# Kernel tuning notes

Measured on AMD Instinct MI355X. Metric: run time of the kernel, lower is better.

Reference implementation:

```python
import jax, jax.numpy as jnp
import numpy as np

E = 8          # num_global_experts
K = 2          # top-k
D = 1024       # model_dim
H = 4096       # hidden_size_per_expert
CAP_FACTOR = 1.0


def setup_inputs() -> dict:
    key = jax.random.key(0)
    ks = jax.random.split(key, 5)
    x = jax.random.normal(ks[0], (4, 2048, D), jnp.float32)
    gate_w = jax.random.normal(ks[1], (E, D), jnp.float32) * 0.02
    fc1_w = jax.random.normal(ks[2], (E, H, D), jnp.float32) * 0.02
    fc1_b = jnp.zeros((E, 1, H), jnp.float32)
    fc2_w = jax.random.normal(ks[3], (E, H, D), jnp.float32) * 0.02
    fc2_b = jnp.zeros((E, 1, D), jnp.float32)
    return {"x": x, "gate_w": gate_w, "fc1_w": fc1_w, "fc1_b": fc1_b,
            "fc2_w": fc2_w, "fc2_b": fc2_b}


def reference(x, gate_w, fc1_w, fc1_b, fc2_w, fc2_b):
    B, S, Dm = x.shape
    xf = x.reshape(-1, Dm)                       # [N, D] tokens
    N = xf.shape[0]
    cap = int(K * CAP_FACTOR * ((N + E - 1) // E))  # expert capacity

    # ---- gating (top-k softmax, normalized) ----
    logits = xf @ gate_w.T                       # [N, E]
    scores = jax.nn.softmax(logits, axis=-1)
    topv, topi = jax.lax.top_k(scores, K)        # [N, K]
    gates = topv / jnp.sum(topv, axis=-1, keepdims=True)

    # ---- per-slot locations within each expert (sequential over K slots) ----
    offset = jnp.zeros((E,), jnp.int32)
    locs = []
    for j in range(K):
        mask = jax.nn.one_hot(topi[:, j], E, dtype=jnp.int32)   # [N, E]
        loc_in = jnp.cumsum(mask, axis=0) - 1 + offset[None, :]
        locs.append(jnp.take_along_axis(loc_in, topi[:, j:j + 1], axis=1)[:, 0])
        offset = offset + mask.sum(axis=0)
    loc = jnp.stack(locs, axis=1)                # [N, K]
    valid = loc < cap                            # capacity-dropped tokens
    flat_idx = jnp.where(valid, topi * cap + loc, 0)   # [N, K]
    w = valid.astype(xf.dtype)

    # ---- dispatch (scatter tokens into [E, cap, D], postscore => unweighted) ----
    disp = jnp.zeros((E * cap, Dm), xf.dtype)
    disp = disp.at[flat_idx.reshape(-1)].add(
        (xf[:, None, :] * w[:, :, None]).reshape(-1, Dm))
    de = disp.reshape(E, cap, Dm)

    # ---- batched expert FFN: relu(x @ fc1^T + b1) @ fc2 + b2 ----
    h = jax.nn.relu(jnp.einsum('ecd,ehd->ech', de, fc1_w) + fc1_b)
    eo = jnp.einsum('ech,ehd->ecd', h, fc2_w) + fc2_b

    # ---- combine (gather + gate-weighted sum over K slots) ----
    gathered = eo.reshape(E * cap, Dm)[flat_idx]       # [N, K, D]
    out = jnp.sum(gathered * (gates * w)[:, :, None], axis=1)
    return out.reshape(B, S, Dm)
```

## Files before the change

kernel.cpp:

```cpp
#include <hip/hip_runtime.h>
#include <hip/hip_bf16.h>
#include <stdint.h>

#define NEXP 8
#define DM   1024
#define HID  4096
#define NTOK 8192
#define CAPS 2048

#define BM 256
#define BN 256
#define BK 64

typedef __attribute__((ext_vector_type(8))) short bh8_t;
typedef __attribute__((ext_vector_type(4))) float f32x4_t;
typedef unsigned short u16;

static __device__ __forceinline__ u16 f2bf(float f) {
    __hip_bfloat16 h = __float2bfloat16(f);
    return __builtin_bit_cast(u16, h);
}
static __device__ __forceinline__ float bf2f(u16 u) {
    unsigned int x = ((unsigned int)u) << 16;
    return __builtin_bit_cast(float, x);
}

#define FENCE asm volatile("" ::: "memory")
#define BAR   do { FENCE; __builtin_amdgcn_s_barrier(); FENCE; } while (0)
#define LGKM0 do { asm volatile("s_waitcnt lgkmcnt(0)" ::: "memory"); \
                   __builtin_amdgcn_sched_barrier(0); } while (0)
#define MFMA(d, a, b) d = __builtin_amdgcn_mfma_f32_16x16x32_bf16(a, b, d, 0, 0, 0)

__global__ __launch_bounds__(256) void k_conv_bf16(const float* __restrict__ in,
                                                   u16* __restrict__ out, long n) {
    long i = ((long)blockIdx.x * 256 + threadIdx.x) * 4;
    if (i >= n) return;
    float4 v = *(const float4*)(in + i);
    ushort4 o;
    o.x = f2bf(v.x); o.y = f2bf(v.y); o.z = f2bf(v.z); o.w = f2bf(v.w);
    *(ushort4*)(out + i) = o;
}

__global__ __launch_bounds__(256) void k_transpose_w2(const float* __restrict__ in,
                                                      u16* __restrict__ out) {
    int e = blockIdx.z;
    const float* I = in + (long)e * HID * DM;
    u16* O = out + (long)e * DM * HID;
    __shared__ float t[32][33];
    int x = threadIdx.x & 31, y = threadIdx.x >> 5;
    int h0 = blockIdx.x * 32, d0 = blockIdx.y * 32;
    #pragma unroll
    for (int i = 0; i < 4; ++i)
        t[y + 8*i][x] = I[(long)(h0 + y + 8*i) * DM + d0 + x];
    __syncthreads();
    #pragma unroll
    for (int i = 0; i < 4; ++i)
        O[(long)(d0 + y + 8*i) * HID + h0 + x] = f2bf(t[x][y + 8*i]);
}

__global__ __launch_bounds__(256) void k_gating(const float* __restrict__ x,
        const float* __restrict__ gw, int* __restrict__ topi, float* __restrict__ gates) {
    __shared__ float sg[NEXP][DM];
    int tid = threadIdx.x;
    for (int i = tid; i < NEXP*DM; i += 256) ((float*)sg)[i] = gw[i];
    __syncthreads();
    int lane = tid & 63, w = tid >> 6;
    long n = (long)blockIdx.x * 4 + w;
    const float* xr = x + n * DM;
    float acc[NEXP] = {};
    for (int i = 0; i < DM/64; ++i) {
        float xv = xr[lane + i*64];
        #pragma unroll
        for (int e = 0; e < NEXP; ++e) acc[e] += xv * sg[e][lane + i*64];
    }
    #pragma unroll
    for (int e = 0; e < NEXP; ++e)
        #pragma unroll
        for (int off = 32; off; off >>= 1) acc[e] += __shfl_xor(acc[e], off);
    if (lane == 0) {
        float mx = acc[0];
        #pragma unroll
        for (int e = 1; e < NEXP; ++e) mx = fmaxf(mx, acc[e]);
        float p[NEXP];
        #pragma unroll
        for (int e = 0; e < NEXP; ++e) p[e] = expf(acc[e] - mx);
        float v0 = p[0]; int i0 = 0;
        #pragma unroll
        for (int e = 1; e < NEXP; ++e) if (p[e] > v0) { v0 = p[e]; i0 = e; }
        float v1 = -1.f; int i1 = 0;
        #pragma unroll
        for (int e = 0; e < NEXP; ++e) if (e != i0 && p[e] > v1) { v1 = p[e]; i1 = e; }
        float tot = v0 + v1;
        topi[n*2]   = i0; topi[n*2+1] = i1;
        gates[n*2]  = v0 / tot; gates[n*2+1] = v1 / tot;
    }
}

__global__ __launch_bounds__(64) void k_locate(const int* __restrict__ topi,
                                               int* __restrict__ flat) {
    int lane = threadIdx.x;
    const int TPL = NTOK / 64;
    int base = lane * TPL;
    int offset[NEXP];
    #pragma unroll
    for (int e = 0; e < NEXP; ++e) offset[e] = 0;
    for (int j = 0; j < 2; ++j) {
        unsigned long long pk = 0;
        for (int t = 0; t < TPL; ++t) {
            int e = topi[(long)(base + t)*2 + j];
            pk += 1ull << (8*e);
        }
        int cnt[NEXP], excl[NEXP];
        #pragma unroll
        for (int e = 0; e < NEXP; ++e) cnt[e] = (int)((pk >> (8*e)) & 0xff);
        #pragma unroll
        for (int e = 0; e < NEXP; ++e) {
            int v = cnt[e];
            for (int d = 1; d < 64; d <<= 1) {
                int o = __shfl_up(v, d);
                if (lane >= d) v += o;
            }
            excl[e] = v - cnt[e] + offset[e];
            offset[e] += __shfl(v, 63);
        }
        unsigned long long lo = 0, hi = 0;
        #pragma unroll
        for (int e = 0; e < 4; ++e)    lo |= (unsigned long long)(excl[e] & 0xffff) << (16*e);
        #pragma unroll
        for (int e = 4; e < NEXP; ++e) hi |= (unsigned long long)(excl[e] & 0xffff) << (16*(e-4));
        for (int t = 0; t < TPL; ++t) {
            long n = base + t;
            int e = topi[n*2 + j];
            int sh = 16 * (e & 3);
            int loc;
            if (e < 4) { loc = (int)((lo >> sh) & 0xffff); lo += 1ull << sh; }
            else       { loc = (int)((hi >> sh) & 0xffff); hi += 1ull << sh; }
            flat[n*2 + j] = (loc < CAPS) ? (e * CAPS + loc) : -1;
        }
    }
}

__global__ __launch_bounds__(256) void k_dispatch(const float* __restrict__ x,
        const int* __restrict__ flat, u16* __restrict__ disp) {
    long n = blockIdx.x;
    int tid = threadIdx.x;
    float4 v = *(const float4*)(x + n*DM + tid*4);
    ushort4 o; o.x = f2bf(v.x); o.y = f2bf(v.y); o.z = f2bf(v.z); o.w = f2bf(v.w);
    int f0 = flat[n*2], f1 = flat[n*2+1];
    if (f0 >= 0) *(ushort4*)(disp + (long)f0*DM + tid*4) = o;
    if (f1 >= 0) *(ushort4*)(disp + (long)f1*DM + tid*4) = o;
}

static __device__ __forceinline__ void stage_half(const u16* __restrict__ g, int ld,
                                                  u16* R, int wid, int lane) {
    int rlo = wid*8 + (lane >> 3);
    int cbe = ((lane & 7) ^ ((lane >> 3) & 7)) * 8;
    const u16* s0 = g + (long)rlo * ld + cbe;
    const u16* s1 = g + (long)(rlo + 64) * ld + cbe;
    u16* d0 = R + wid*512 + lane*8;
    u16* d1 = R + 4096 + wid*512 + lane*8;
    __builtin_amdgcn_global_load_lds((const __attribute__((address_space(1))) void*)s0,
        (__attribute__((address_space(3))) void*)d0, 16, 0, 0);
    __builtin_amdgcn_global_load_lds((const __attribute__((address_space(1))) void*)s1,
        (__attribute__((address_space(3))) void*)d1, 16, 0, 0);
}

template<int RELU>
__global__ __launch_bounds__(512, 2)
void k_gemm8(const u16* __restrict__ A, const u16* __restrict__ B,
             const float* __restrict__ bias, u16* __restrict__ C,
             int N, int K, long strA, long strB, long strBias, long strC)
{
    __shared__ u16 sm[2][2][2][8192];

    int gx = gridDim.x, gy = gridDim.y;
    int nwg = gx * gy * (int)gridDim.z;
    int lin = blockIdx.x + gx * (blockIdx.y + gy * blockIdx.z);
    int qq  = nwg >> 3;
    int swz = (lin & 7) * qq + (lin >> 3);
    int gxy = gx * gy;
    int bz = swz / gxy, rm = swz % gxy, by = rm / gx, bx = rm % gx;

    const u16* Ae = A + (long)bz * strA;
    const u16* Be = B + (long)bz * strB;
    const float* bi = bias + (long)bz * strBias;
    u16* Ce = C + (long)bz * strC;

    long tm = (long)by * BM, tn = (long)bx * BN;
    const u16* Abase = Ae + tm * (long)K;
    const u16* Bbase = Be + tn * (long)K;

    int tid = threadIdx.x, lane = tid & 63, wid = tid >> 6;
    int wr = wid >> 2, wc = wid & 3;

    int frow = lane & 15;
    int fc0 = (((lane >> 4) * 16)      ^ ((lane & 7) << 4)) >> 1;
    int fc1 = ((64 + (lane >> 4) * 16) ^ ((lane & 7) << 4)) >> 1;

    const int NT = K / BK;

    f32x4_t acc[8][4] = {};

    auto STG = [&](int buf, int ab, int half, int kt) {
        const u16* g = (ab ? Bbase : Abase) + (long)(half * 128) * K + (long)kt * BK;
        stage_half(g, K, &sm[buf][ab][half][0], wid, lane);
    };
    auto LDA = [&](int c, int mi, int kk) -> bh8_t {
        const u16* p = &sm[c][0][wr][0] + (mi * 16 + frow) * 64 + (kk ? fc1 : fc0);
        return *(const bh8_t*)p;
    };
    auto LDB = [&](int c, int ni, int kk) -> bh8_t {
        const u16* p = &sm[c][1][wc >> 1][0] + ((wc & 1) * 64 + ni * 16 + frow) * 64 + (kk ? fc1 : fc0);
        return *(const bh8_t*)p;
    };

    auto ktile = [&](int c, int kt, int s12, int s34, int vm) {
        bh8_t a0[4][2], a1[4][2], bf[4][2];
        #pragma unroll
        for (int mi = 0; mi < 4; ++mi) { a0[mi][0] = LDA(c, mi, 0); a0[mi][1] = LDA(c, mi, 1); }
        #pragma unroll
        for (int ni = 0; ni < 2; ++ni) { bf[ni][0] = LDB(c, ni, 0); bf[ni][1] = LDB(c, ni, 1); }
        if (s12) STG(c ^ 1, 0, 1, kt + 1);
        BAR; LGKM0;
        __builtin_amdgcn_s_setprio(1);
        #pragma unroll
        for (int mi = 0; mi < 4; ++mi)
            #pragma unroll
            for (int ni = 0; ni < 2; ++ni)
                #pragma unroll
                for (int kk = 0; kk < 2; ++kk) MFMA(acc[mi][ni], a0[mi][kk], bf[ni][kk]);
        __builtin_amdgcn_s_setprio(0);
        __builtin_amdgcn_sched_barrier(0);
        BAR;
        #pragma unroll
        for (int ni = 2; ni < 4; ++ni) { bf[ni][0] = LDB(c, ni, 0); bf[ni][1] = LDB(c, ni, 1); }
        if (s12) STG(c ^ 1, 1, 1, kt + 1);
        BAR; LGKM0;
        __builtin_amdgcn_s_setprio(1);
        #pragma unroll
        for (int mi = 0; mi < 4; ++mi)
            #pragma unroll
            for (int ni = 2; ni < 4; ++ni)
                #pragma unroll
                for (int kk = 0; kk < 2; ++kk) MFMA(acc[mi][ni], a0[mi][kk], bf[ni][kk]);
        __builtin_amdgcn_s_setprio(0);
        __builtin_amdgcn_sched_barrier(0);
        BAR;
        #pragma unroll
        for (int mi = 0; mi < 4; ++mi) { a1[mi][0] = LDA(c, mi + 4, 0); a1[mi][1] = LDA(c, mi + 4, 1); }
        if (s34) STG(c, 1, 0, kt + 2);
        BAR; LGKM0;
        __builtin_amdgcn_s_setprio(1);
        #pragma unroll
        for (int mi = 0; mi < 4; ++mi)
            #pragma unroll
            for (int ni = 0; ni < 2; ++ni)
                #pragma unroll
                for (int kk = 0; kk < 2; ++kk) MFMA(acc[mi + 4][ni], a1[mi][kk], bf[ni][kk]);
        __builtin_amdgcn_s_setprio(0);
        __builtin_amdgcn_sched_barrier(0);
        BAR;
        if (s34) STG(c, 0, 0, kt + 2);
        if (vm == 4)      { asm volatile("s_waitcnt vmcnt(4)" ::: "memory"); }
        else if (vm == 0) { asm volatile("s_waitcnt vmcnt(0)" ::: "memory"); }
        BAR; LGKM0;
        __builtin_amdgcn_s_setprio(1);
        #pragma unroll
        for (int mi = 0; mi < 4; ++mi)
            #pragma unroll
            for (int ni = 2; ni < 4; ++ni)
                #pragma unroll
                for (int kk = 0; kk < 2; ++kk) MFMA(acc[mi + 4][ni], a1[mi][kk], bf[ni][kk]);
        __builtin_amdgcn_s_setprio(0);
        __builtin_amdgcn_sched_barrier(0);
        BAR;
    };

    STG(0, 0, 0, 0); STG(0, 0, 1, 0); STG(0, 1, 0, 0); STG(0, 1, 1, 0);
    STG(1, 1, 0, 1); STG(1, 0, 0, 1);
    asm volatile("s_waitcnt vmcnt(4)" ::: "memory");
    BAR;

    int kt = 0;
    for (; kt < NT - 2; ++kt) ktile(kt & 1, kt, 1, 1, 4);
    ktile(kt & 1, kt, 1, 0, 0); ++kt;
    ktile(kt & 1, kt, 0, 0, -1);

    u16* wb = &sm[0][0][0][0] + wid * 8192;
    #pragma unroll
    for (int mi = 0; mi < 8; ++mi)
        #pragma unroll
        for (int ni = 0; ni < 4; ++ni) {
            float bv = bi[tn + wc * 64 + ni * 16 + (lane & 15)];
            #pragma unroll
            for (int r = 0; r < 4; ++r) {
                int row = mi * 16 + (lane >> 4) * 4 + r;
                int ce  = ni * 16 + (lane & 15);
                float v = acc[mi][ni][r] + bv;
                if (RELU) v = fmaxf(v, 0.f);
                wb[row * 64 + (ce ^ ((row & 7) << 3))] = f2bf(v);
            }
        }
    __syncthreads();
    long crow = tm + wr * 128;
    long ccol = tn + wc * 64 + (lane & 7) * 8;
    #pragma unroll
    for (int i = 0; i < 16; ++i) {
        int rr = i * 8 + (lane >> 3);
        bh8_t v = *(const bh8_t*)(wb + rr * 64 + (((lane & 7) * 8) ^ ((rr & 7) << 3)));
        *(bh8_t*)(Ce + (crow + rr) * N + ccol) = v;
    }
}

__global__ __launch_bounds__(256) void k_combine(const u16* __restrict__ eo,
        const int* __restrict__ flat, const float* __restrict__ gates,
        float* __restrict__ out) {
    long n = blockIdx.x;
    int tid = threadIdx.x;
    int f0 = flat[n*2], f1 = flat[n*2+1];
    float g0 = (f0 >= 0) ? gates[n*2]   : 0.f;
    float g1 = (f1 >= 0) ? gates[n*2+1] : 0.f;
    const u16* r0 = eo + (long)(f0 >= 0 ? f0 : 0) * DM;
    const u16* r1 = eo + (long)(f1 >= 0 ? f1 : 0) * DM;
    ushort4 a = *(const ushort4*)(r0 + tid*4);
    ushort4 b = *(const ushort4*)(r1 + tid*4);
    float4 o;
    o.x = g0*bf2f(a.x) + g1*bf2f(b.x);
    o.y = g0*bf2f(a.y) + g1*bf2f(b.y);
    o.z = g0*bf2f(a.z) + g1*bf2f(b.z);
    o.w = g0*bf2f(a.w) + g1*bf2f(b.w);
    *(float4*)(out + n*DM + tid*4) = o;
}

extern "C" void kernel_launch(void* const* d_in, const int* in_sizes, int n_in,
                              void* d_out, int out_size, void* d_ws, size_t ws_size,
                              hipStream_t stream) {
    const float* x    = (const float*)d_in[0];
    const float* gw   = (const float*)d_in[1];
    const float* fc1w = (const float*)d_in[2];
    const float* fc1b = (const float*)d_in[3];
    const float* fc2w = (const float*)d_in[4];
    const float* fc2b = (const float*)d_in[5];
    float* out = (float*)d_out;
    char* ws = (char*)d_ws;

    u16* disp = (u16*)(ws);
    u16* eo   = disp;
    u16* h    = (u16*)(ws + 33554432L);
    u16* w1b  = (u16*)(ws + 33554432L + 134217728L);
    u16* w2t  = (u16*)(ws + 33554432L + 134217728L + 67108864L);
    char* tail = ws + 33554432L + 134217728L + 67108864L + 67108864L;
    int*   topi  = (int*)tail;
    float* gates = (float*)(tail + 65536);
    int*   flat  = (int*)(tail + 131072);

    long n1 = (long)NEXP * HID * DM;

    hipMemsetAsync(disp, 0, (size_t)NEXP * CAPS * DM * 2, stream);
    k_conv_bf16<<<dim3(n1/1024), 256, 0, stream>>>(fc1w, w1b, n1);
    k_transpose_w2<<<dim3(HID/32, DM/32, NEXP), 256, 0, stream>>>(fc2w, w2t);
    k_gating<<<dim3(NTOK/4), 256, 0, stream>>>(x, gw, topi, gates);
    k_locate<<<dim3(1), 64, 0, stream>>>(topi, flat);
    k_dispatch<<<dim3(NTOK), 256, 0, stream>>>(x, flat, disp);
    k_gemm8<1><<<dim3(HID/BN, CAPS/BM, NEXP), 512, 0, stream>>>(
        disp, w1b, fc1b, h, HID, DM,
        (long)CAPS*DM, (long)HID*DM, (long)HID, (long)CAPS*HID);
    k_gemm8<0><<<dim3(DM/BN, CAPS/BM, NEXP), 512, 0, stream>>>(
        h, w2t, fc2b, eo, DM, HID,
        (long)CAPS*HID, (long)DM*HID, (long)DM, (long)CAPS*DM);
    k_combine<<<dim3(NTOK), 256, 0, stream>>>(eo, flat, gates, out);
}
```

Before: 471.9 us.

## Fuse fc1 weight bf16 conversion into GEMM loads, widen transpose, drop memset

Removes the standalone fp32-to-bf16 conversion pass over fc1 weights. The first expert GEMM now loads fp32 B tiles into registers, converts them, and writes them swizzled into LDS within a reworked software pipeline. The fc2 transpose kernel moves to 64x64 tiles with float4 loads and 16-byte bf16 stores, and the zeroing memset of the dispatch buffer is dropped. In exchange, GEMM1 reads twice the B bytes for every tile it reuses across row blocks and adds conversion ALU work and register pressure. It also relies on never-gathered capacity slots not mattering.

```diff
diff --git a/kernel.cpp b/kernel.cpp
--- a/kernel.cpp
+++ b/kernel.cpp
@@ -29,33 +29,36 @@
 #define BAR   do { FENCE; __builtin_amdgcn_s_barrier(); FENCE; } while (0)
 #define LGKM0 do { asm volatile("s_waitcnt lgkmcnt(0)" ::: "memory"); \
                    __builtin_amdgcn_sched_barrier(0); } while (0)
+#define SB0   __builtin_amdgcn_sched_barrier(0)
 #define MFMA(d, a, b) d = __builtin_amdgcn_mfma_f32_16x16x32_bf16(a, b, d, 0, 0, 0)
-
-__global__ __launch_bounds__(256) void k_conv_bf16(const float* __restrict__ in,
-                                                   u16* __restrict__ out, long n) {
-    long i = ((long)blockIdx.x * 256 + threadIdx.x) * 4;
-    if (i >= n) return;
-    float4 v = *(const float4*)(in + i);
-    ushort4 o;
-    o.x = f2bf(v.x); o.y = f2bf(v.y); o.z = f2bf(v.z); o.w = f2bf(v.w);
-    *(ushort4*)(out + i) = o;
-}
 
 __global__ __launch_bounds__(256) void k_transpose_w2(const float* __restrict__ in,
                                                       u16* __restrict__ out) {
     int e = blockIdx.z;
     const float* I = in + (long)e * HID * DM;
     u16* O = out + (long)e * DM * HID;
-    __shared__ float t[32][33];
-    int x = threadIdx.x & 31, y = threadIdx.x >> 5;
-    int h0 = blockIdx.x * 32, d0 = blockIdx.y * 32;
-    #pragma unroll
-    for (int i = 0; i < 4; ++i)
-        t[y + 8*i][x] = I[(long)(h0 + y + 8*i) * DM + d0 + x];
+    __shared__ float t[64][65];
+    int h0 = blockIdx.x * 64, d0 = blockIdx.y * 64;
+    int tid = threadIdx.x;
+    int r = tid >> 4, cw = (tid & 15) * 4;
+    #pragma unroll
+    for (int i = 0; i < 4; ++i) {
+        float4 v = *(const float4*)(I + (long)(h0 + r + 16*i) * DM + d0 + cw);
+        t[r + 16*i][cw]     = v.x;
+        t[r + 16*i][cw + 1] = v.y;
+        t[r + 16*i][cw + 2] = v.z;
+        t[r + 16*i][cw + 3] = v.w;
+    }
     __syncthreads();
-    #pragma unroll
-    for (int i = 0; i < 4; ++i)
-        O[(long)(d0 + y + 8*i) * HID + h0 + x] = f2bf(t[x][y + 8*i]);
+    int dl = tid >> 2, hc = (tid & 3) * 16;
+    bh8_t w0, w1;
+    #pragma unroll
+    for (int j = 0; j < 8; ++j) w0[j] = (short)f2bf(t[hc + j][dl]);
+    #pragma unroll
+    for (int j = 0; j < 8; ++j) w1[j] = (short)f2bf(t[hc + 8 + j][dl]);
+    u16* o = O + (long)(d0 + dl) * HID + h0 + hc;
+    *(bh8_t*)o = w0;
+    *(bh8_t*)(o + 8) = w1;
 }
 
 __global__ __launch_bounds__(256) void k_gating(const float* __restrict__ x,
@@ -165,9 +168,11 @@
         (__attribute__((address_space(3))) void*)d1, 16, 0, 0);
 }
 
-template<int RELU>
+struct Bregs { float4 a0, a1, b0, b1; };
+
+template<int RELU, int BF32>
 __global__ __launch_bounds__(512, 2)
-void k_gemm8(const u16* __restrict__ A, const u16* __restrict__ B,
+void k_gemm8(const u16* __restrict__ A, const void* __restrict__ Bv,
              const float* __restrict__ bias, u16* __restrict__ C,
              int N, int K, long strA, long strB, long strBias, long strC)
 {
@@ -182,13 +187,15 @@
     int bz = swz / gxy, rm = swz % gxy, by = rm / gx, bx = rm % gx;
 
     const u16* Ae = A + (long)bz * strA;
-    const u16* Be = B + (long)bz * strB;
     const float* bi = bias + (long)bz * strBias;
     u16* Ce = C + (long)bz * strC;
 
     long tm = (long)by * BM, tn = (long)bx * BN;
     const u16* Abase = Ae + tm * (long)K;
-    const u16* Bbase = Be + tn * (long)K;
+    const u16*   Bbase16 = nullptr;
+    const float* Bbase32 = nullptr;
+    if constexpr (BF32) Bbase32 = (const float*)Bv + (long)bz * strB + tn * (long)K;
+    else                Bbase16 = (const u16*)Bv  + (long)bz * strB + tn * (long)K;
 
     int tid = threadIdx.x, lane = tid & 63, wid = tid >> 6;
     int wr = wid >> 2, wc = wid & 3;
@@ -197,13 +204,36 @@
     int fc0 = (((lane >> 4) * 16)      ^ ((lane & 7) << 4)) >> 1;
     int fc1 = ((64 + (lane >> 4) * 16) ^ ((lane & 7) << 4)) >> 1;
 
+    int rlo = wid*8 + (lane >> 3);
+    int c0  = (lane & 7) * 8;
+
     const int NT = K / BK;
 
     f32x4_t acc[8][4] = {};
 
     auto STG = [&](int buf, int ab, int half, int kt) {
-        const u16* g = (ab ? Bbase : Abase) + (long)(half * 128) * K + (long)kt * BK;
+        const u16* g = (ab ? Bbase16 : Abase) + (long)(half * 128) * K + (long)kt * BK;
         stage_half(g, K, &sm[buf][ab][half][0], wid, lane);
+    };
+    auto LBLD = [&](int half, int kt) -> Bregs {
+        const float* g  = Bbase32 + (long)(half * 128 + rlo) * K + (long)kt * BK + c0;
+        const float* g2 = g + 64L * K;
+        Bregs r;
+        r.a0 = *(const float4*)g;  r.a1 = *(const float4*)(g + 4);
+        r.b0 = *(const float4*)g2; r.b1 = *(const float4*)(g2 + 4);
+        return r;
+    };
+    auto BWR = [&](int buf, int half, const Bregs& v) {
+        u16* R = &sm[buf][1][half][0];
+        int key = (rlo & 7) << 3;
+        u16* d1 = R + rlo * 64 + (c0 ^ key);
+        u16* d2 = R + (rlo + 64) * 64 + (c0 ^ key);
+        bh8_t w1, w2;
+        w1[0]=(short)f2bf(v.a0.x); w1[1]=(short)f2bf(v.a0.y); w1[2]=(short)f2bf(v.a0.z); w1[3]=(short)f2bf(v.a0.w);
+        w1[4]=(short)f2bf(v.a1.x); w1[5]=(short)f2bf(v.a1.y); w1[6]=(short)f2bf(v.a1.z); w1[7]=(short)f2bf(v.a1.w);
+        w2[0]=(short)f2bf(v.b0.x); w2[1]=(short)f2bf(v.b0.y); w2[2]=(short)f2bf(v.b0.z); w2[3]=(short)f2bf(v.b0.w);
+        w2[4]=(short)f2bf(v.b1.x); w2[5]=(short)f2bf(v.b1.y); w2[6]=(short)f2bf(v.b1.z); w2[7]=(short)f2bf(v.b1.w);
+        *(bh8_t*)d1 = w1; *(bh8_t*)d2 = w2;
     };
     auto LDA = [&](int c, int mi, int kk) -> bh8_t {
         const u16* p = &sm[c][0][wr][0] + (mi * 16 + frow) * 64 + (kk ? fc1 : fc0);
@@ -214,7 +244,7 @@
         return *(const bh8_t*)p;
     };
 
-    auto ktile = [&](int c, int kt, int s12, int s34, int vm) {
+    auto ktile16 = [&](int c, int kt, int s12, int s34, int vm) {
         bh8_t a0[4][2], a1[4][2], bf[4][2];
         #pragma unroll
         for (int mi = 0; mi < 4; ++mi) { a0[mi][0] = LDA(c, mi, 0); a0[mi][1] = LDA(c, mi, 1); }
@@ -229,9 +259,7 @@
             for (int ni = 0; ni < 2; ++ni)
                 #pragma unroll
                 for (int kk = 0; kk < 2; ++kk) MFMA(acc[mi][ni], a0[mi][kk], bf[ni][kk]);
-        __builtin_amdgcn_s_setprio(0);
-        __builtin_amdgcn_sched_barrier(0);
-        BAR;
+        __builtin_amdgcn_s_setprio(0); SB0; BAR;
         #pragma unroll
         for (int ni = 2; ni < 4; ++ni) { bf[ni][0] = LDB(c, ni, 0); bf[ni][1] = LDB(c, ni, 1); }
         if (s12) STG(c ^ 1, 1, 1, kt + 1);
@@ -243,9 +271,7 @@
             for (int ni = 2; ni < 4; ++ni)
                 #pragma unroll
                 for (int kk = 0; kk < 2; ++kk) MFMA(acc[mi][ni], a0[mi][kk], bf[ni][kk]);
-        __builtin_amdgcn_s_setprio(0);
-        __builtin_amdgcn_sched_barrier(0);
-        BAR;
+        __builtin_amdgcn_s_setprio(0); SB0; BAR;
         #pragma unroll
         for (int mi = 0; mi < 4; ++mi) { a1[mi][0] = LDA(c, mi + 4, 0); a1[mi][1] = LDA(c, mi + 4, 1); }
         if (s34) STG(c, 1, 0, kt + 2);
@@ -257,9 +283,7 @@
             for (int ni = 0; ni < 2; ++ni)
                 #pragma unroll
                 for (int kk = 0; kk < 2; ++kk) MFMA(acc[mi + 4][ni], a1[mi][kk], bf[ni][kk]);
-        __builtin_amdgcn_s_setprio(0);
-        __builtin_amdgcn_sched_barrier(0);
-        BAR;
+        __builtin_amdgcn_s_setprio(0); SB0; BAR;
         if (s34) STG(c, 0, 0, kt + 2);
         if (vm == 4)      { asm volatile("s_waitcnt vmcnt(4)" ::: "memory"); }
         else if (vm == 0) { asm volatile("s_waitcnt vmcnt(0)" ::: "memory"); }
@@ -271,20 +295,105 @@
             for (int ni = 2; ni < 4; ++ni)
                 #pragma unroll
                 for (int kk = 0; kk < 2; ++kk) MFMA(acc[mi + 4][ni], a1[mi][kk], bf[ni][kk]);
-        __builtin_amdgcn_s_setprio(0);
-        __builtin_amdgcn_sched_barrier(0);
+        __builtin_amdgcn_s_setprio(0); SB0; BAR;
+    };
+
+    auto ktile32 = [&](int c, int kt, int s12, int s34) {
+        bh8_t a0[4][2], a1[4][2], bf[4][2];
+        Bregs lb1, lb0;
+        #pragma unroll
+        for (int mi = 0; mi < 4; ++mi) { a0[mi][0] = LDA(c, mi, 0); a0[mi][1] = LDA(c, mi, 1); }
+        #pragma unroll
+        for (int ni = 0; ni < 2; ++ni) { bf[ni][0] = LDB(c, ni, 0); bf[ni][1] = LDB(c, ni, 1); }
+        SB0;
+        if (s12) lb1 = LBLD(1, kt + 1);
+        SB0;
+        if (s34) lb0 = LBLD(0, kt + 2);
+        SB0;
+        if (s12) STG(c ^ 1, 0, 1, kt + 1);
+        BAR; LGKM0;
+        __builtin_amdgcn_s_setprio(1);
+        #pragma unroll
+        for (int mi = 0; mi < 4; ++mi)
+            #pragma unroll
+            for (int ni = 0; ni < 2; ++ni)
+                #pragma unroll
+                for (int kk = 0; kk < 2; ++kk) MFMA(acc[mi][ni], a0[mi][kk], bf[ni][kk]);
+        __builtin_amdgcn_s_setprio(0); SB0; BAR;
+        #pragma unroll
+        for (int ni = 2; ni < 4; ++ni) { bf[ni][0] = LDB(c, ni, 0); bf[ni][1] = LDB(c, ni, 1); }
+        BAR; LGKM0;
+        __builtin_amdgcn_s_setprio(1);
+        #pragma unroll
+        for (int mi = 0; mi < 4; ++mi)
+            #pragma unroll
+            for (int ni = 2; ni < 4; ++ni)
+                #pragma unroll
+                for (int kk = 0; kk < 2; ++kk) MFMA(acc[mi][ni], a0[mi][kk], bf[ni][kk]);
+        __builtin_amdgcn_s_setprio(0); SB0; BAR;
+        #pragma unroll
+        for (int mi = 0; mi < 4; ++mi) { a1[mi][0] = LDA(c, mi + 4, 0); a1[mi][1] = LDA(c, mi + 4, 1); }
+        SB0;
+        if (s12) {
+            if (s34) { asm volatile("s_waitcnt vmcnt(6)" ::: "memory"); }
+            else     { asm volatile("s_waitcnt vmcnt(2)" ::: "memory"); }
+            BWR(c ^ 1, 1, lb1);
+        }
+        BAR; LGKM0;
+        __builtin_amdgcn_s_setprio(1);
+        #pragma unroll
+        for (int mi = 0; mi < 4; ++mi)
+            #pragma unroll
+            for (int ni = 0; ni < 2; ++ni)
+                #pragma unroll
+                for (int kk = 0; kk < 2; ++kk) MFMA(acc[mi + 4][ni], a1[mi][kk], bf[ni][kk]);
+        __builtin_amdgcn_s_setprio(0); SB0; BAR;
+        if (s34) {
+            asm volatile("s_waitcnt vmcnt(2)" ::: "memory");
+            BWR(c, 0, lb0);
+            SB0;
+            STG(c, 0, 0, kt + 2);
+            SB0;
+        }
+        if (s12) {
+            if (s34) { asm volatile("s_waitcnt vmcnt(2)" ::: "memory"); }
+            else     { asm volatile("s_waitcnt vmcnt(0)" ::: "memory"); }
+        }
+        BAR; LGKM0;
+        __builtin_amdgcn_s_setprio(1);
+        #pragma unroll
+        for (int mi = 0; mi < 4; ++mi)
+            #pragma unroll
+            for (int ni = 2; ni < 4; ++ni)
+                #pragma unroll
+                for (int kk = 0; kk < 2; ++kk) MFMA(acc[mi + 4][ni], a1[mi][kk], bf[ni][kk]);
+        __builtin_amdgcn_s_setprio(0); SB0; BAR;
+    };
+
+    if constexpr (BF32) {
+        Bregs t0 = LBLD(0, 0);
+        asm volatile("s_waitcnt vmcnt(0)" ::: "memory"); BWR(0, 0, t0);
+        Bregs t1 = LBLD(1, 0);
+        asm volatile("s_waitcnt vmcnt(0)" ::: "memory"); BWR(0, 1, t1);
+        Bregs t2 = LBLD(0, 1);
+        asm volatile("s_waitcnt vmcnt(0)" ::: "memory"); BWR(1, 0, t2);
+        STG(0, 0, 0, 0); STG(0, 0, 1, 0); STG(1, 0, 0, 1);
+        asm volatile("s_waitcnt vmcnt(0) lgkmcnt(0)" ::: "memory");
         BAR;
-    };
-
-    STG(0, 0, 0, 0); STG(0, 0, 1, 0); STG(0, 1, 0, 0); STG(0, 1, 1, 0);
-    STG(1, 1, 0, 1); STG(1, 0, 0, 1);
-    asm volatile("s_waitcnt vmcnt(4)" ::: "memory");
-    BAR;
-
-    int kt = 0;
-    for (; kt < NT - 2; ++kt) ktile(kt & 1, kt, 1, 1, 4);
-    ktile(kt & 1, kt, 1, 0, 0); ++kt;
-    ktile(kt & 1, kt, 0, 0, -1);
+        int kt = 0;
+        for (; kt < NT - 2; ++kt) ktile32(kt & 1, kt, 1, 1);
+        ktile32(kt & 1, kt, 1, 0); ++kt;
+        ktile32(kt & 1, kt, 0, 0);
+    } else {
+        STG(0, 0, 0, 0); STG(0, 0, 1, 0); STG(0, 1, 0, 0); STG(0, 1, 1, 0);
+        STG(1, 1, 0, 1); STG(1, 0, 0, 1);
+        asm volatile("s_waitcnt vmcnt(4)" ::: "memory");
+        BAR;
+        int kt = 0;
+        for (; kt < NT - 2; ++kt) ktile16(kt & 1, kt, 1, 1, 4);
+        ktile16(kt & 1, kt, 1, 0, 0); ++kt;
+        ktile16(kt & 1, kt, 0, 0, -1);
+    }
 
     u16* wb = &sm[0][0][0][0] + wid * 8192;
     #pragma unroll
@@ -347,26 +456,21 @@
     u16* disp = (u16*)(ws);
     u16* eo   = disp;
     u16* h    = (u16*)(ws + 33554432L);
-    u16* w1b  = (u16*)(ws + 33554432L + 134217728L);
-    u16* w2t  = (u16*)(ws + 33554432L + 134217728L + 67108864L);
-    char* tail = ws + 33554432L + 134217728L + 67108864L + 67108864L;
+    u16* w2t  = (u16*)(ws + 33554432L + 134217728L);
+    char* tail = ws + 33554432L + 134217728L + 67108864L;
     int*   topi  = (int*)tail;
     float* gates = (float*)(tail + 65536);
     int*   flat  = (int*)(tail + 131072);
 
-    long n1 = (long)NEXP * HID * DM;
-
-    hipMemsetAsync(disp, 0, (size_t)NEXP * CAPS * DM * 2, stream);
-    k_conv_bf16<<<dim3(n1/1024), 256, 0, stream>>>(fc1w, w1b, n1);
-    k_transpose_w2<<<dim3(HID/32, DM/32, NEXP), 256, 0, stream>>>(fc2w, w2t);
+    k_transpose_w2<<<dim3(HID/64, DM/64, NEXP), 256, 0, stream>>>(fc2w, w2t);
     k_gating<<<dim3(NTOK/4), 256, 0, stream>>>(x, gw, topi, gates);
     k_locate<<<dim3(1), 64, 0, stream>>>(topi, flat);
     k_dispatch<<<dim3(NTOK), 256, 0, stream>>>(x, flat, disp);
-    k_gemm8<1><<<dim3(HID/BN, CAPS/BM, NEXP), 512, 0, stream>>>(
-        disp, w1b, fc1b, h, HID, DM,
+    k_gemm8<1, 1><<<dim3(HID/BN, CAPS/BM, NEXP), 512, 0, stream>>>(
+        disp, (const void*)fc1w, fc1b, h, HID, DM,
         (long)CAPS*DM, (long)HID*DM, (long)HID, (long)CAPS*HID);
-    k_gemm8<0><<<dim3(DM/BN, CAPS/BM, NEXP), 512, 0, stream>>>(
-        h, w2t, fc2b, eo, DM, HID,
+    k_gemm8<0, 0><<<dim3(DM/BN, CAPS/BM, NEXP), 512, 0, stream>>>(
+        h, (const void*)w2t, fc2b, eo, DM, HID,
         (long)CAPS*HID, (long)DM*HID, (long)DM, (long)CAPS*DM);
     k_combine<<<dim3(NTOK), 256, 0, stream>>>(eo, flat, gates, out);
 }
```

New measurement: 487.4 us. 1.03x slower.
